# Performance work log

Measured on AMD Instinct MI355X. Metric: run time of the kernel, lower is better.

Reference implementation:

```python
import jax, jax.numpy as jnp
import numpy as np

B, S, D, H = 4, 2048, 1024, 16
HD = D // H
DFF = 4 * D
NUM_LAYERS = 12
RES = 1.0 / float(np.sqrt(NUM_LAYERS))
SCALE = 1.0 / float(np.sqrt(D))  # module divides by sqrt(embed_dim), not head_dim
EPS = 1e-5


def setup_inputs() -> dict:
    key = jax.random.key(0)
    ks = jax.random.split(key, 12)
    s = 0.02
    p = lambda k, shp: (jax.random.normal(k, shp, jnp.float32) * s)
    return {
        "x": jax.random.normal(ks[0], (B, S, D), jnp.float32),
        "Wq": p(ks[1], (D, D)), "bq": jnp.zeros((D,), jnp.float32),
        "Wk": p(ks[2], (D, D)), "bk": jnp.zeros((D,), jnp.float32),
        "Wv": p(ks[3], (D, D)), "bv": jnp.zeros((D,), jnp.float32),
        "Wo": p(ks[4], (D, D)), "bo": jnp.zeros((D,), jnp.float32),
        "g1": jnp.ones((D,), jnp.float32), "be1": jnp.zeros((D,), jnp.float32),
        "g2": jnp.ones((D,), jnp.float32), "be2": jnp.zeros((D,), jnp.float32),
        "W1": p(ks[5], (D, DFF)), "b1": jnp.zeros((DFF,), jnp.float32),
        "W2": p(ks[6], (DFF, D)), "b2": jnp.zeros((D,), jnp.float32),
    }


def _layernorm(x, g, b):
    m = jnp.mean(x, axis=-1, keepdims=True)
    v = jnp.mean((x - m) ** 2, axis=-1, keepdims=True)
    return (x - m) * jax.lax.rsqrt(v + EPS) * g + b


def _attention(x, Wq, bq, Wk, bk, Wv, bv, Wo, bo):
    b, s, d = x.shape
    q = (x @ Wq + bq).reshape(b, s, H, HD)
    k = (x @ Wk + bk).reshape(b, s, H, HD)
    v = (x @ Wv + bv).reshape(b, s, H, HD)
    scores = jnp.einsum('bqhd,bkhd->bhqk', q, k) * SCALE  # [B,H,S,S]
    mask = jnp.tril(jnp.ones((s, s), dtype=bool))
    scores = jnp.where(mask, scores, -jnp.inf)
    attn = jax.nn.softmax(scores, axis=-1)  # dropout_rate=0 -> identity
    out = jnp.einsum('bhqk,bkhd->bqhd', attn, v).reshape(b, s, d)
    return out @ Wo + bo


def reference(x, Wq, bq, Wk, bk, Wv, bv, Wo, bo, g1, be1, g2, be2, W1, b1, W2, b2):
    x = x + RES * _attention(_layernorm(x, g1, be1), Wq, bq, Wk, bk, Wv, bv, Wo, bo)
    h = _layernorm(x, g2, be2)
    ffn = jax.nn.relu(h @ W1 + b1) @ W2 + b2
    x = x + RES * ffn
    return x
```

## Files before the change

kernel.cpp:

```cpp
#include <hip/hip_runtime.h>

typedef unsigned short ushort_t;
typedef unsigned int uint32;
typedef __attribute__((ext_vector_type(4))) float f32x4;
typedef __attribute__((ext_vector_type(8))) short bf16x8;

#define B_   4
#define S_   2048
#define D_   1024
#define H_   16
#define HD_  64
#define DFF_ 4096
#define M_   (B_ * S_)

#define RES_   0.28867513459481287f
#define SCALE_ 0.03125f
#define EPS_   1e-5f
#define LOG2E_ 1.4426950408889634f

__device__ __forceinline__ ushort_t f2bf(float f) {
    union { float f; uint32 u; } c; c.f = f;
    uint32 u = c.u + 0x7fffu + ((c.u >> 16) & 1u);
    return (ushort_t)(u >> 16);
}
__device__ __forceinline__ float bf2f(ushort_t h) {
    union { uint32 u; float f; } c; c.u = ((uint32)h) << 16;
    return c.f;
}
__device__ __forceinline__ float fexp2(float x) {
    float r; asm("v_exp_f32 %0, %1" : "=v"(r) : "v"(x)); return r;
}
__device__ __forceinline__ uint32 cvt_pk_bf16(float lo, float hi) {
    uint32 r;
    asm("v_cvt_pk_bf16_f32 %0, %1, %2" : "=v"(r) : "v"(lo), "v"(hi));
    return r;
}

#define GLDS(src_, dst_)                                                     \
    __builtin_amdgcn_global_load_lds(                                        \
        (const __attribute__((address_space(1))) void*)(src_),               \
        (__attribute__((address_space(3))) void*)(dst_), 16, 0, 0)

__global__ __launch_bounds__(256) void transpose_cast_kernel(
    const float* __restrict__ W, ushort_t* __restrict__ Wt, int K, int N)
{
    __shared__ float tile[32][33];
    const int bx = blockIdx.x * 32;
    const int by = blockIdx.y * 32;
    const int tx = threadIdx.x;
    const int ty = threadIdx.y;
    #pragma unroll
    for (int i = 0; i < 32; i += 8)
        tile[ty + i][tx] = W[(size_t)(by + ty + i) * N + bx + tx];
    __syncthreads();
    #pragma unroll
    for (int i = 0; i < 32; i += 8)
        Wt[(size_t)(bx + ty + i) * K + by + tx] = f2bf(tile[tx][ty + i]);
}

__global__ void concat_bias_kernel(const float* __restrict__ bq,
                                   const float* __restrict__ bk,
                                   const float* __restrict__ bv,
                                   float* __restrict__ bqkv)
{
    int i = blockIdx.x * blockDim.x + threadIdx.x;
    if (i < 3 * D_) {
        float v = (i < D_) ? bq[i] : (i < 2 * D_) ? bk[i - D_] : bv[i - 2 * D_];
        bqkv[i] = v;
    }
}

__global__ __launch_bounds__(256) void ln_kernel(
    const float* __restrict__ x, const float* __restrict__ g,
    const float* __restrict__ be, ushort_t* __restrict__ out)
{
    const int row = blockIdx.x;
    const int t = threadIdx.x;
    const int lane = t & 63;
    const int wave = t >> 6;
    const float4* xr = (const float4*)(x + (size_t)row * D_);
    float4 v = xr[t];
    float s  = v.x + v.y + v.z + v.w;
    float s2 = v.x * v.x + v.y * v.y + v.z * v.z + v.w * v.w;
    #pragma unroll
    for (int off = 32; off; off >>= 1) {
        s  += __shfl_xor(s, off);
        s2 += __shfl_xor(s2, off);
    }
    __shared__ float red[8];
    if (lane == 0) { red[wave * 2] = s; red[wave * 2 + 1] = s2; }
    __syncthreads();
    s  = red[0] + red[2] + red[4] + red[6];
    s2 = red[1] + red[3] + red[5] + red[7];
    const float mean = s * (1.0f / D_);
    const float var  = s2 * (1.0f / D_) - mean * mean;
    const float rstd = rsqrtf(var + EPS_);
    const float4 gv  = ((const float4*)g)[t];
    const float4 bv  = ((const float4*)be)[t];
    ushort_t o[4];
    o[0] = f2bf((v.x - mean) * rstd * gv.x + bv.x);
    o[1] = f2bf((v.y - mean) * rstd * gv.y + bv.y);
    o[2] = f2bf((v.z - mean) * rstd * gv.z + bv.z);
    o[3] = f2bf((v.w - mean) * rstd * gv.w + bv.w);
    *(ushort2*)&out[(size_t)row * D_ + t * 4]     = make_ushort2(o[0], o[1]);
    *(ushort2*)&out[(size_t)row * D_ + t * 4 + 2] = make_ushort2(o[2], o[3]);
}

__global__ __launch_bounds__(256) void vtrans_kernel(
    const ushort_t* __restrict__ qkv, ushort_t* __restrict__ vt)
{
    __shared__ __align__(16) ushort_t T[256 * 64];
    const int tid  = threadIdx.x;
    const int sblk = blockIdx.x & 7;
    const int bh   = blockIdx.x >> 3;
    const int b = bh >> 4, h = bh & 15;
    const ushort_t* src = qkv + (size_t)(b * S_ + sblk * 256) * (3 * D_) + 2 * D_ + h * 64;
    #pragma unroll
    for (int p = 0; p < 8; ++p) {
        const int L = p * 256 + tid;
        const int s = L >> 3, c = L & 7;
        bf16x8 v = *(const bf16x8*)(src + (size_t)s * (3 * D_) + c * 8);
        *(bf16x8*)&T[s * 64 + ((c ^ (s & 7)) << 3)] = v;
    }
    __syncthreads();
    #pragma unroll
    for (int p = 0; p < 8; ++p) {
        const int L = p * 256 + tid;
        const int hd = L >> 5, scn = L & 31;
        ushort_t tmp[8];
        #pragma unroll
        for (int j = 0; j < 8; ++j) {
            const int s = scn * 8 + j;
            tmp[j] = T[s * 64 + (((hd >> 3) ^ (s & 7)) << 3) + (hd & 7)];
        }
        *(bf16x8*)&vt[((size_t)bh * 64 + hd) * S_ + sblk * 256 + scn * 8] =
            *(const bf16x8*)tmp;
    }
}

template <int MODE>
__global__ __launch_bounds__(512, 1) void gemm8p_kernel(
    const ushort_t* __restrict__ A, const ushort_t* __restrict__ Bt,
    const float* __restrict__ bias, const float* __restrict__ res,
    void* __restrict__ Cout, int M, int N, int K, int gx)
{
    __shared__ __align__(16) ushort_t As[2][256 * 64];
    __shared__ __align__(16) ushort_t Bs[2][256 * 64];

    const int tid  = threadIdx.x;
    const int w    = tid >> 6;
    const int lane = tid & 63;
    const int l15  = lane & 15;
    const int g    = lane >> 4;

    const int cpx = gridDim.x >> 3;
    const int swz = (blockIdx.x & 7) * cpx + (blockIdx.x >> 3);
    const int bx = swz % gx, by = swz / gx;
    const int m0 = by * 256, n0 = bx * 256;

    const int wm = (w >> 2) * 128;
    const int wn = (w & 3) * 64;

    const ushort_t* srcA[4];
    const ushort_t* srcB[4];
    int ldsO[4];
    #pragma unroll
    for (int p = 0; p < 4; ++p) {
        const int L = p * 512 + tid;
        const int row = L >> 3;
        const int c = ((L & 7) ^ (row & 7)) << 3;
        srcA[p] = A  + (size_t)(m0 + row) * K + c;
        srcB[p] = Bt + (size_t)(n0 + row) * K + c;
        ldsO[p] = (p * 512 + w * 64) * 8;
    }

    #define LDA(mf_, kk_) (*(const bf16x8*)&As[cur][(wm + (mf_) * 16 + l15) * 64 + \
                  (((((kk_) * 4 + g)) ^ ((wm + (mf_) * 16 + l15) & 7)) << 3)])
    #define LDB(nf_, kk_) (*(const bf16x8*)&Bs[cur][(wn + (nf_) * 16 + l15) * 64 + \
                  (((((kk_) * 4 + g)) ^ ((wn + (nf_) * 16 + l15) & 7)) << 3)])
    #define MM4(base_)                                                         \
        do { _Pragma("unroll")                                                 \
             for (int mf = 0; mf < 4; ++mf)                                    \
                 _Pragma("unroll")                                             \
                 for (int nf = 0; nf < 4; ++nf)                                \
                     acc[(base_) + mf][nf] =                                   \
                         __builtin_amdgcn_mfma_f32_16x16x32_bf16(              \
                             af[mf], bfr[nf], acc[(base_) + mf][nf], 0, 0, 0); \
        } while (0)

    f32x4 acc[8][4] = {};
    const int NT = K >> 6;

    #pragma unroll
    for (int p = 0; p < 4; ++p) GLDS(srcA[p], &As[0][ldsO[p]]);
    #pragma unroll
    for (int p = 0; p < 4; ++p) GLDS(srcB[p], &Bs[0][ldsO[p]]);
    asm volatile("s_waitcnt vmcnt(0)" ::: "memory");
    __builtin_amdgcn_s_barrier();

    for (int t = 0; t < NT; ++t) {
        const int cur = t & 1;
        const int nb  = cur ^ 1;
        const bool more = (t + 1 < NT);
        const size_t koff = (size_t)(t + 1) * 64;

        bf16x8 af[4], bfr[4];

        #pragma unroll
        for (int nf = 0; nf < 4; ++nf) bfr[nf] = LDB(nf, 0);
        #pragma unroll
        for (int mf = 0; mf < 4; ++mf) af[mf] = LDA(mf, 0);
        if (more) {
            #pragma unroll
            for (int p = 0; p < 4; ++p) GLDS(srcA[p] + koff, &As[nb][ldsO[p]]);
        }
        __builtin_amdgcn_s_barrier();
        __builtin_amdgcn_s_setprio(1);
        MM4(0);
        __builtin_amdgcn_s_setprio(0);
        __builtin_amdgcn_s_barrier();

        #pragma unroll
        for (int mf = 0; mf < 4; ++mf) af[mf] = LDA(mf + 4, 0);
        if (more) {
            #pragma unroll
            for (int p = 0; p < 4; ++p) GLDS(srcB[p] + koff, &Bs[nb][ldsO[p]]);
        }
        __builtin_amdgcn_s_barrier();
        __builtin_amdgcn_s_setprio(1);
        MM4(4);
        __builtin_amdgcn_s_setprio(0);
        __builtin_amdgcn_s_barrier();

        #pragma unroll
        for (int nf = 0; nf < 4; ++nf) bfr[nf] = LDB(nf, 1);
        #pragma unroll
        for (int mf = 0; mf < 4; ++mf) af[mf] = LDA(mf, 1);
        __builtin_amdgcn_s_barrier();
        __builtin_amdgcn_s_setprio(1);
        MM4(0);
        __builtin_amdgcn_s_setprio(0);
        __builtin_amdgcn_s_barrier();

        #pragma unroll
        for (int mf = 0; mf < 4; ++mf) af[mf] = LDA(mf + 4, 1);
        __builtin_amdgcn_s_setprio(1);
        MM4(4);
        __builtin_amdgcn_s_setprio(0);
        asm volatile("s_waitcnt vmcnt(0)" ::: "memory");
        __builtin_amdgcn_s_barrier();
    }
    #undef LDA
    #undef LDB
    #undef MM4

    const int rbase = g * 4;
    #pragma unroll
    for (int mf = 0; mf < 8; ++mf) {
        #pragma unroll
        for (int nf = 0; nf < 4; ++nf) {
            const int col = n0 + wn + nf * 16 + l15;
            const float bcol = bias[col];
            #pragma unroll
            for (int r = 0; r < 4; ++r) {
                const int row = m0 + wm + mf * 16 + rbase + r;
                float v = acc[mf][nf][r] + bcol;
                const size_t idx = (size_t)row * N + col;
                if (MODE == 0) {
                    ((ushort_t*)Cout)[idx] = f2bf(v);
                } else if (MODE == 1) {
                    ((ushort_t*)Cout)[idx] = f2bf(fmaxf(v, 0.0f));
                } else {
                    ((float*)Cout)[idx] = res[idx] + RES_ * v;
                }
            }
        }
    }
}

template <int MODE>
__global__ __launch_bounds__(512, 2) void gemmT_kernel(
    const ushort_t* __restrict__ A, const ushort_t* __restrict__ Bt,
    const float* __restrict__ bias, const float* __restrict__ res,
    void* __restrict__ Cout, int M, int N, int K, int gx)
{
    constexpr int LOADS = 3;

    __shared__ __align__(16) ushort_t As[3][128 * 32];
    __shared__ __align__(16) ushort_t Bs[3][256 * 32];

    const int tid  = threadIdx.x;
    const int w    = tid >> 6;
    const int lane = tid & 63;
    const int l15  = lane & 15;
    const int g    = lane >> 4;

    const int cpx = gridDim.x >> 3;
    const int swz = (blockIdx.x & 7) * cpx + (blockIdx.x >> 3);
    const int bx = swz % gx, by = swz / gx;
    const int m0 = by * 128, n0 = bx * 256;

    const int wm = (w >> 2) * 64;
    const int wn = (w & 3) * 64;

    const ushort_t* srcA;
    int ldsA;
    const ushort_t* srcB[2];
    int ldsB[2];
    {
        const int L = tid;
        const int row = L >> 2;
        srcA = A + (size_t)(m0 + row) * K + (((L & 3) ^ ((row >> 1) & 3)) << 3);
        ldsA = (w * 64) * 8;
    }
    #pragma unroll
    for (int p = 0; p < 2; ++p) {
        const int L = p * 512 + tid;
        const int row = L >> 2;
        srcB[p] = Bt + (size_t)(n0 + row) * K + (((L & 3) ^ ((row >> 1) & 3)) << 3);
        ldsB[p] = (p * 512 + w * 64) * 8;
    }

    #define STAGE(koff_, buf_)                                               \
        do {                                                                 \
            GLDS(srcA + (koff_), &As[buf_][ldsA]);                           \
            GLDS(srcB[0] + (koff_), &Bs[buf_][ldsB[0]]);                     \
            GLDS(srcB[1] + (koff_), &Bs[buf_][ldsB[1]]);                     \
        } while (0)

    #define LDA(mf_) (*(const bf16x8*)&As[cur][(wm + (mf_) * 16 + l15) * 32 + \
                        ((g ^ (((wm + (mf_) * 16 + l15) >> 1) & 3)) << 3)])
    #define LDB(nf_) (*(const bf16x8*)&Bs[cur][(wn + (nf_) * 16 + l15) * 32 + \
                        ((g ^ (((wn + (nf_) * 16 + l15) >> 1) & 3)) << 3)])

    f32x4 acc[4][4] = {};
    const int NT = K >> 5;

    STAGE(0, 0);
    STAGE(32, 1);
    asm volatile("s_waitcnt vmcnt(%0)" :: "n"(LOADS) : "memory");
    __builtin_amdgcn_s_barrier();

    for (int t = 0; t < NT; ++t) {
        const int cur = t % 3;
        const bool more = (t + 2 < NT);
        const size_t koff = (size_t)(t + 2) * 32;

        bf16x8 af[4], bfr[4];
        #pragma unroll
        for (int nf = 0; nf < 4; ++nf) bfr[nf] = LDB(nf);
        #pragma unroll
        for (int mf = 0; mf < 4; ++mf) af[mf] = LDA(mf);

        if (more) STAGE(koff, (t + 2) % 3);
        __builtin_amdgcn_s_setprio(1);
        #pragma unroll
        for (int mf = 0; mf < 4; ++mf)
            #pragma unroll
            for (int nf = 0; nf < 4; ++nf)
                acc[mf][nf] = __builtin_amdgcn_mfma_f32_16x16x32_bf16(
                    af[mf], bfr[nf], acc[mf][nf], 0, 0, 0);
        __builtin_amdgcn_s_setprio(0);
        if (more)
            asm volatile("s_waitcnt vmcnt(%0)" :: "n"(LOADS) : "memory");
        else
            asm volatile("s_waitcnt vmcnt(0)" ::: "memory");
        __builtin_amdgcn_s_barrier();
    }
    #undef STAGE
    #undef LDA
    #undef LDB

    const int rbase = g * 4;
    #pragma unroll
    for (int mf = 0; mf < 4; ++mf) {
        #pragma unroll
        for (int nf = 0; nf < 4; ++nf) {
            const int col = n0 + wn + nf * 16 + l15;
            const float bcol = bias[col];
            #pragma unroll
            for (int r = 0; r < 4; ++r) {
                const int row = m0 + wm + mf * 16 + rbase + r;
                float v = acc[mf][nf][r] + bcol;
                const size_t idx = (size_t)row * N + col;
                if (MODE == 0) {
                    ((ushort_t*)Cout)[idx] = f2bf(v);
                } else if (MODE == 1) {
                    ((ushort_t*)Cout)[idx] = f2bf(fmaxf(v, 0.0f));
                } else {
                    ((float*)Cout)[idx] = res[idx] + RES_ * v;
                }
            }
        }
    }
}

__global__ __launch_bounds__(256) void fattn_kernel(
    const ushort_t* __restrict__ qkv, const ushort_t* __restrict__ vtg,
    ushort_t* __restrict__ out)
{
    __shared__ __align__(16) ushort_t Ks[2][64 * 64];
    __shared__ __align__(16) ushort_t Vt[2][64 * 64];
    __shared__ __align__(16) ushort_t Ps[4][16 * 64];

    const int tid  = threadIdx.x;
    const int lane = tid & 63;
    const int w    = tid >> 6;
    const int lin  = blockIdx.x;
    const int xi   = lin >> 6;
    const int bh   = lin & 63;
    const int b = bh >> 4, h = bh & 15;

    const int l15 = lane & 15;
    const int g   = lane >> 4;

    const size_t rs = 3 * D_;
    const ushort_t* Qg = qkv + (size_t)b * S_ * rs + h * HD_;
    const ushort_t* Kg = Qg + D_;
    const ushort_t* Vg = vtg + (size_t)bh * HD_ * S_;

    const int srow = tid >> 3;
    const int sc   = tid & 7;

    #pragma unroll
    for (int half = 0; half < 2; ++half) {
        const int qt = half ? xi : (S_ / 64 - 1) - xi;
        const int q0 = qt * 64;
        const int nkb = qt + 1;

        bf16x8 qf[2];
        {
            const int qrow = q0 + w * 16 + l15;
            #pragma unroll
            for (int kk = 0; kk < 2; ++kk) {
                bf16x8 tq = *(const bf16x8*)(Qg + (size_t)qrow * rs + kk * 32 + g * 8);
                #pragma unroll
                for (int e = 0; e < 8; ++e)
                    tq[e] = (short)f2bf(bf2f((ushort_t)tq[e]) * (SCALE_ * LOG2E_));
                qf[kk] = tq;
            }
        }

        float mrow = -1e30f, lrow = 0.f;
        f32x4 oacc[4] = {};

        bf16x8 kvreg[2][2], vvreg[2][2];
        #pragma unroll
        for (int p = 0; p < 2; ++p) {
            const int row = p * 32 + srow;
            kvreg[0][p] = *(const bf16x8*)(Kg + (size_t)row * rs + sc * 8);
            vvreg[0][p] = *(const bf16x8*)(Vg + (size_t)row * S_ + sc * 8);
        }
        if (nkb > 1) {
            #pragma unroll
            for (int p = 0; p < 2; ++p) {
                const int row = p * 32 + srow;
                kvreg[1][p] = *(const bf16x8*)(Kg + (size_t)(64 + row) * rs + sc * 8);
                vvreg[1][p] = *(const bf16x8*)(Vg + (size_t)row * S_ + 64 + sc * 8);
            }
        }

        int kb = 0;
        for (; kb + 1 < nkb; kb += 2) {
            __syncthreads();
            #pragma unroll
            for (int s = 0; s < 2; ++s)
                #pragma unroll
                for (int p = 0; p < 2; ++p) {
                    const int row = p * 32 + srow;
                    *(bf16x8*)&Ks[s][row * 64 + ((sc ^ (row & 7)) << 3)] = kvreg[s][p];
                    *(bf16x8*)&Vt[s][row * 64 + ((sc ^ (row & 7)) << 3)] = vvreg[s][p];
                }
            if (kb + 2 < nkb) {
                #pragma unroll
                for (int p = 0; p < 2; ++p) {
                    const int row = p * 32 + srow;
                    kvreg[0][p] = *(const bf16x8*)(
                        Kg + (size_t)((kb + 2) * 64 + row) * rs + sc * 8);
                    vvreg[0][p] = *(const bf16x8*)(
                        Vg + (size_t)row * S_ + (kb + 2) * 64 + sc * 8);
                }
            }
            if (kb + 3 < nkb) {
                #pragma unroll
                for (int p = 0; p < 2; ++p) {
                    const int row = p * 32 + srow;
                    kvreg[1][p] = *(const bf16x8*)(
                        Kg + (size_t)((kb + 3) * 64 + row) * rs + sc * 8);
                    vvreg[1][p] = *(const bf16x8*)(
                        Vg + (size_t)row * S_ + (kb + 3) * 64 + sc * 8);
                }
            }
            __syncthreads();

            f32x4 sf0[4] = {}, sf1[4] = {};
            __builtin_amdgcn_s_setprio(1);
            #pragma unroll
            for (int kk = 0; kk < 2; ++kk) {
                const int cc = kk * 4 + g;
                #pragma unroll
                for (int nf = 0; nf < 4; ++nf) {
                    const int keyr = nf * 16 + l15;
                    const int ko = keyr * 64 + ((cc ^ (keyr & 7)) << 3);
                    bf16x8 kf0 = *(const bf16x8*)&Ks[0][ko];
                    bf16x8 kf1 = *(const bf16x8*)&Ks[1][ko];
                    sf0[nf] = __builtin_amdgcn_mfma_f32_16x16x32_bf16(kf0, qf[kk], sf0[nf], 0, 0, 0);
                    sf1[nf] = __builtin_amdgcn_mfma_f32_16x16x32_bf16(kf1, qf[kk], sf1[nf], 0, 0, 0);
                }
            }
            __builtin_amdgcn_s_setprio(0);

            if (kb + 1 == nkb - 1) {
                const int q = q0 + w * 16 + l15;
                #pragma unroll
                for (int nf = 0; nf < 4; ++nf)
                    #pragma unroll
                    for (int r = 0; r < 4; ++r)
                        if ((kb + 1) * 64 + nf * 16 + g * 4 + r > q) sf1[nf][r] = -1e30f;
            }

            float mx = -1e30f;
            #pragma unroll
            for (int nf = 0; nf < 4; ++nf)
                #pragma unroll
                for (int r = 0; r < 4; ++r) {
                    mx = fmaxf(mx, sf0[nf][r]);
                    mx = fmaxf(mx, sf1[nf][r]);
                }
            mx = fmaxf(mx, __shfl_xor(mx, 16));
            mx = fmaxf(mx, __shfl_xor(mx, 32));

            if (!__all(mx - mrow <= 8.0f)) {
                const float mnew = fmaxf(mrow, mx);
                const float corr = fexp2(mrow - mnew);
                mrow = mnew;
                lrow *= corr;
                #pragma unroll
                for (int r = 0; r < 4; ++r) {
                    const float cr = __shfl(corr, g * 4 + r, 16);
                    #pragma unroll
                    for (int nf = 0; nf < 4; ++nf) oacc[nf][r] *= cr;
                }
            }

            float psum = 0.f;
            const int qrow = l15;
            #pragma unroll
            for (int s = 0; s < 2; ++s) {
                const f32x4* sfp = s ? sf1 : sf0;
                #pragma unroll
                for (int nf = 0; nf < 4; ++nf) {
                    const float p0 = fexp2(sfp[nf][0] - mrow);
                    const float p1 = fexp2(sfp[nf][1] - mrow);
                    const float p2 = fexp2(sfp[nf][2] - mrow);
                    const float p3 = fexp2(sfp[nf][3] - mrow);
                    psum += (p0 + p1) + (p2 + p3);
                    uint2 pk = make_uint2(cvt_pk_bf16(p0, p1), cvt_pk_bf16(p2, p3));
                    const int c16 = ((nf << 1) + (g >> 1)) ^ (qrow & 7);
                    *(uint2*)((char*)Ps[w] + qrow * 128 + c16 * 16 + (g & 1) * 8) = pk;
                }
                #pragma unroll
                for (int kk = 0; kk < 2; ++kk) {
                    const int cc = kk * 4 + g;
                    const int c16 = cc ^ (qrow & 7);
                    bf16x8 pa = *(const bf16x8*)((const char*)Ps[w] + qrow * 128 + c16 * 16);
                    __builtin_amdgcn_s_setprio(1);
                    #pragma unroll
                    for (int nf = 0; nf < 4; ++nf) {
                        const int dr = nf * 16 + l15;
                        bf16x8 vf = *(const bf16x8*)&Vt[s][dr * 64 + ((cc ^ (dr & 7)) << 3)];
                        oacc[nf] = __builtin_amdgcn_mfma_f32_16x16x32_bf16(pa, vf, oacc[nf], 0, 0, 0);
                    }
                    __builtin_amdgcn_s_setprio(0);
                }
            }
            psum += __shfl_xor(psum, 16);
            psum += __shfl_xor(psum, 32);
            lrow += psum;
        }

        if (kb < nkb) {
            __syncthreads();
            #pragma unroll
            for (int p = 0; p < 2; ++p) {
                const int row = p * 32 + srow;
                *(bf16x8*)&Ks[0][row * 64 + ((sc ^ (row & 7)) << 3)] = kvreg[0][p];
                *(bf16x8*)&Vt[0][row * 64 + ((sc ^ (row & 7)) << 3)] = vvreg[0][p];
            }
            __syncthreads();

            f32x4 sf0[4] = {};
            __builtin_amdgcn_s_setprio(1);
            #pragma unroll
            for (int kk = 0; kk < 2; ++kk) {
                const int cc = kk * 4 + g;
                #pragma unroll
                for (int nf = 0; nf < 4; ++nf) {
                    const int keyr = nf * 16 + l15;
                    bf16x8 kf = *(const bf16x8*)&Ks[0][keyr * 64 + ((cc ^ (keyr & 7)) << 3)];
                    sf0[nf] = __builtin_amdgcn_mfma_f32_16x16x32_bf16(kf, qf[kk], sf0[nf], 0, 0, 0);
                }
            }
            __builtin_amdgcn_s_setprio(0);

            {
                const int q = q0 + w * 16 + l15;
                #pragma unroll
                for (int nf = 0; nf < 4; ++nf)
                    #pragma unroll
                    for (int r = 0; r < 4; ++r)
                        if (kb * 64 + nf * 16 + g * 4 + r > q) sf0[nf][r] = -1e30f;
            }
            float mx = -1e30f;
            #pragma unroll
            for (int nf = 0; nf < 4; ++nf)
                #pragma unroll
                for (int r = 0; r < 4; ++r) mx = fmaxf(mx, sf0[nf][r]);
            mx = fmaxf(mx, __shfl_xor(mx, 16));
            mx = fmaxf(mx, __shfl_xor(mx, 32));

            if (!__all(mx - mrow <= 8.0f)) {
                const float mnew = fmaxf(mrow, mx);
                const float corr = fexp2(mrow - mnew);
                mrow = mnew;
                lrow *= corr;
                #pragma unroll
                for (int r = 0; r < 4; ++r) {
                    const float cr = __shfl(corr, g * 4 + r, 16);
                    #pragma unroll
                    for (int nf = 0; nf < 4; ++nf) oacc[nf][r] *= cr;
                }
            }

            float psum = 0.f;
            const int qrow = l15;
            #pragma unroll
            for (int nf = 0; nf < 4; ++nf) {
                const float p0 = fexp2(sf0[nf][0] - mrow);
                const float p1 = fexp2(sf0[nf][1] - mrow);
                const float p2 = fexp2(sf0[nf][2] - mrow);
                const float p3 = fexp2(sf0[nf][3] - mrow);
                psum += (p0 + p1) + (p2 + p3);
                uint2 pk = make_uint2(cvt_pk_bf16(p0, p1), cvt_pk_bf16(p2, p3));
                const int c16 = ((nf << 1) + (g >> 1)) ^ (qrow & 7);
                *(uint2*)((char*)Ps[w] + qrow * 128 + c16 * 16 + (g & 1) * 8) = pk;
            }
            psum += __shfl_xor(psum, 16);
            psum += __shfl_xor(psum, 32);
            lrow += psum;

            #pragma unroll
            for (int kk = 0; kk < 2; ++kk) {
                const int cc = kk * 4 + g;
                const int c16 = cc ^ (qrow & 7);
                bf16x8 pa = *(const bf16x8*)((const char*)Ps[w] + qrow * 128 + c16 * 16);
                __builtin_amdgcn_s_setprio(1);
                #pragma unroll
                for (int nf = 0; nf < 4; ++nf) {
                    const int dr = nf * 16 + l15;
                    bf16x8 vf = *(const bf16x8*)&Vt[0][dr * 64 + ((cc ^ (dr & 7)) << 3)];
                    oacc[nf] = __builtin_amdgcn_mfma_f32_16x16x32_bf16(pa, vf, oacc[nf], 0, 0, 0);
                }
                __builtin_amdgcn_s_setprio(0);
            }
        }

        const float linv = 1.0f / lrow;
        #pragma unroll
        for (int r = 0; r < 4; ++r) {
            const float li = __shfl(linv, g * 4 + r, 16);
            const int q = q0 + w * 16 + g * 4 + r;
            ushort_t* op = out + (size_t)(b * S_ + q) * D_ + h * HD_;
            #pragma unroll
            for (int nf = 0; nf < 4; ++nf)
                op[nf * 16 + l15] = f2bf(oacc[nf][r] * li);
        }
    }
}

extern "C" void kernel_launch(void* const* d_in, const int* in_sizes, int n_in,
                              void* d_out, int out_size, void* d_ws, size_t ws_size,
                              hipStream_t stream)
{
    const float* x   = (const float*)d_in[0];
    const float* Wq  = (const float*)d_in[1];
    const float* bq  = (const float*)d_in[2];
    const float* Wk  = (const float*)d_in[3];
    const float* bk  = (const float*)d_in[4];
    const float* Wv  = (const float*)d_in[5];
    const float* bv  = (const float*)d_in[6];
    const float* Wo  = (const float*)d_in[7];
    const float* bo  = (const float*)d_in[8];
    const float* g1  = (const float*)d_in[9];
    const float* be1 = (const float*)d_in[10];
    const float* g2  = (const float*)d_in[11];
    const float* be2 = (const float*)d_in[12];
    const float* W1  = (const float*)d_in[13];
    const float* b1  = (const float*)d_in[14];
    const float* W2  = (const float*)d_in[15];
    const float* b2  = (const float*)d_in[16];
    float* out = (float*)d_out;

    char* ws = (char*)d_ws;
    size_t o = 0;
    auto alloc = [&](size_t bytes) { size_t r = o; o = (o + bytes + 255) & ~(size_t)255; return r; };
    ushort_t* Wqkvt = (ushort_t*)(ws + alloc((size_t)3 * D_ * D_ * 2));
    ushort_t* Wot   = (ushort_t*)(ws + alloc((size_t)D_ * D_ * 2));
    ushort_t* W1t   = (ushort_t*)(ws + alloc((size_t)DFF_ * D_ * 2));
    ushort_t* W2t   = (ushort_t*)(ws + alloc((size_t)D_ * DFF_ * 2));
    float*    bqkv  = (float*)(ws + alloc((size_t)3 * D_ * 4));
    ushort_t* lnbuf = (ushort_t*)(ws + alloc((size_t)M_ * D_ * 2));
    ushort_t* bigbuf= (ushort_t*)(ws + alloc((size_t)M_ * DFF_ * 2));
    ushort_t* attnb = (ushort_t*)(ws + alloc((size_t)M_ * D_ * 2));
    float*    x1    = (float*)(ws + alloc((size_t)M_ * D_ * 4));
    ushort_t* vtbuf = (ushort_t*)(ws + alloc((size_t)M_ * D_ * 2));

    dim3 tblock(32, 8);
    transpose_cast_kernel<<<dim3(D_/32, D_/32), tblock, 0, stream>>>(Wq, Wqkvt,            D_, D_);
    transpose_cast_kernel<<<dim3(D_/32, D_/32), tblock, 0, stream>>>(Wk, Wqkvt + D_*D_,    D_, D_);
    transpose_cast_kernel<<<dim3(D_/32, D_/32), tblock, 0, stream>>>(Wv, Wqkvt + 2*D_*D_,  D_, D_);
    transpose_cast_kernel<<<dim3(D_/32, D_/32), tblock, 0, stream>>>(Wo, Wot,              D_, D_);
    transpose_cast_kernel<<<dim3(DFF_/32, D_/32), tblock, 0, stream>>>(W1, W1t,            D_, DFF_);
    transpose_cast_kernel<<<dim3(D_/32, DFF_/32), tblock, 0, stream>>>(W2, W2t,            DFF_, D_);
    concat_bias_kernel<<<12, 256, 0, stream>>>(bq, bk, bv, bqkv);

    ln_kernel<<<M_, 256, 0, stream>>>(x, g1, be1, lnbuf);
    gemm8p_kernel<0><<<(M_/256)*(3*D_/256), 512, 0, stream>>>(
        lnbuf, Wqkvt, bqkv, nullptr, bigbuf, M_, 3*D_, D_, 3*D_/256);
    vtrans_kernel<<<512, 256, 0, stream>>>(bigbuf, vtbuf);
    fattn_kernel<<<(S_/128) * 64, 256, 0, stream>>>(bigbuf, vtbuf, attnb);
    gemmT_kernel<2><<<(M_/128)*(D_/256), 512, 0, stream>>>(
        attnb, Wot, bo, x, x1, M_, D_, D_, D_/256);
    ln_kernel<<<M_, 256, 0, stream>>>(x1, g2, be2, lnbuf);
    gemm8p_kernel<1><<<(M_/256)*(DFF_/256), 512, 0, stream>>>(
        lnbuf, W1t, b1, nullptr, bigbuf, M_, DFF_, D_, DFF_/256);
    gemmT_kernel<2><<<(M_/128)*(D_/256), 512, 0, stream>>>(
        bigbuf, W2t, b2, x1, out, M_, D_, DFF_, D_/256);
}
```

Baseline: 386.2 us.

## Split GEMM LDS tiles into half-blocks and spread prefetch across four phases

Result: no change. 391.4 us (+1.3%).

```diff
diff --git a/kernel.cpp b/kernel.cpp
--- a/kernel.cpp
+++ b/kernel.cpp
@@ -139,13 +139,13 @@
 }
 
 template <int MODE>
-__global__ __launch_bounds__(512, 1) void gemm8p_kernel(
+__global__ __launch_bounds__(512, 1) void gemm8v_kernel(
     const ushort_t* __restrict__ A, const ushort_t* __restrict__ Bt,
     const float* __restrict__ bias, const float* __restrict__ res,
     void* __restrict__ Cout, int M, int N, int K, int gx)
 {
-    __shared__ __align__(16) ushort_t As[2][256 * 64];
-    __shared__ __align__(16) ushort_t Bs[2][256 * 64];
+    __shared__ __align__(16) ushort_t LdsA[4 * 128 * 64];
+    __shared__ __align__(16) ushort_t LdsB[4 * 128 * 64];
 
     const int tid  = threadIdx.x;
     const int w    = tid >> 6;
@@ -158,26 +158,41 @@
     const int bx = swz % gx, by = swz / gx;
     const int m0 = by * 256, n0 = bx * 256;
 
-    const int wm = (w >> 2) * 128;
+    const int ah = w >> 2;
+    const int bh = (w & 3) >> 1;
+    const int wm = ah * 128;
     const int wn = (w & 3) * 64;
 
     const ushort_t* srcA[4];
     const ushort_t* srcB[4];
-    int ldsO[4];
+    int dstA[4], dstB[4];
     #pragma unroll
     for (int p = 0; p < 4; ++p) {
-        const int L = p * 512 + tid;
-        const int row = L >> 3;
-        const int c = ((L & 7) ^ (row & 7)) << 3;
-        srcA[p] = A  + (size_t)(m0 + row) * K + c;
-        srcB[p] = Bt + (size_t)(n0 + row) * K + c;
-        ldsO[p] = (p * 512 + w * 64) * 8;
-    }
-
-    #define LDA(mf_, kk_) (*(const bf16x8*)&As[cur][(wm + (mf_) * 16 + l15) * 64 + \
-                  (((((kk_) * 4 + g)) ^ ((wm + (mf_) * 16 + l15) & 7)) << 3)])
-    #define LDB(nf_, kk_) (*(const bf16x8*)&Bs[cur][(wn + (nf_) * 16 + l15) * 64 + \
-                  (((((kk_) * 4 + g)) ^ ((wn + (nf_) * 16 + l15) & 7)) << 3)])
+        {
+            const int chunk = (w & 3) * 64 + p * 256 + lane;
+            const int rl = chunk >> 3;
+            srcA[p] = A + (size_t)(m0 + ah * 128 + rl) * K +
+                      (((chunk & 7) ^ (rl & 7)) << 3);
+            dstA[p] = ((w & 3) * 64 + p * 256) * 8;
+        }
+        {
+            const int chunk = ((w >> 2) * 2 + (w & 1)) * 64 + p * 256 + lane;
+            const int rl = chunk >> 3;
+            srcB[p] = Bt + (size_t)(n0 + bh * 128 + rl) * K +
+                      (((chunk & 7) ^ (rl & 7)) << 3);
+            dstB[p] = (((w >> 2) * 2 + (w & 1)) * 64 + p * 256) * 8;
+        }
+    }
+
+    #define SLOTA(t_) ((((t_) & 1) * 2 + ah) * 8192)
+    #define SLOTB(t_) ((((t_) & 1) * 2 + bh) * 8192)
+    #define STG_A(t_, p_)  GLDS(srcA[p_] + (size_t)(t_) * 64, &LdsA[SLOTA(t_) + dstA[p_]])
+    #define STG_B(t_, p_)  GLDS(srcB[p_] + (size_t)(t_) * 64, &LdsB[SLOTB(t_) + dstB[p_]])
+
+    #define LDA(mf_, kk_) (*(const bf16x8*)&LdsA[cA + ((mf_) * 16 + l15) * 64 + \
+                              ((((kk_) * 4 + g) ^ (l15 & 7)) << 3)])
+    #define LDB(nf_, kk_) (*(const bf16x8*)&LdsB[cB + ((w & 1) * 64 + (nf_) * 16 + l15) * 64 + \
+                              ((((kk_) * 4 + g) ^ (l15 & 7)) << 3)])
     #define MM4(base_)                                                         \
         do { _Pragma("unroll")                                                 \
              for (int mf = 0; mf < 4; ++mf)                                    \
@@ -192,17 +207,16 @@
     const int NT = K >> 6;
 
     #pragma unroll
-    for (int p = 0; p < 4; ++p) GLDS(srcA[p], &As[0][ldsO[p]]);
-    #pragma unroll
-    for (int p = 0; p < 4; ++p) GLDS(srcB[p], &Bs[0][ldsO[p]]);
+    for (int p = 0; p < 4; ++p) STG_A(0, p);
+    #pragma unroll
+    for (int p = 0; p < 4; ++p) STG_B(0, p);
     asm volatile("s_waitcnt vmcnt(0)" ::: "memory");
     __builtin_amdgcn_s_barrier();
 
     for (int t = 0; t < NT; ++t) {
-        const int cur = t & 1;
-        const int nb  = cur ^ 1;
+        const int cA = SLOTA(t);
+        const int cB = SLOTB(t);
         const bool more = (t + 1 < NT);
-        const size_t koff = (size_t)(t + 1) * 64;
 
         bf16x8 af[4], bfr[4];
 
@@ -210,10 +224,7 @@
         for (int nf = 0; nf < 4; ++nf) bfr[nf] = LDB(nf, 0);
         #pragma unroll
         for (int mf = 0; mf < 4; ++mf) af[mf] = LDA(mf, 0);
-        if (more) {
-            #pragma unroll
-            for (int p = 0; p < 4; ++p) GLDS(srcA[p] + koff, &As[nb][ldsO[p]]);
-        }
+        if (more) { STG_A(t + 1, 0); STG_A(t + 1, 1); }
         __builtin_amdgcn_s_barrier();
         __builtin_amdgcn_s_setprio(1);
         MM4(0);
@@ -222,10 +233,7 @@
 
         #pragma unroll
         for (int mf = 0; mf < 4; ++mf) af[mf] = LDA(mf + 4, 0);
-        if (more) {
-            #pragma unroll
-            for (int p = 0; p < 4; ++p) GLDS(srcB[p] + koff, &Bs[nb][ldsO[p]]);
-        }
+        if (more) { STG_A(t + 1, 2); STG_A(t + 1, 3); }
         __builtin_amdgcn_s_barrier();
         __builtin_amdgcn_s_setprio(1);
         MM4(4);
@@ -236,6 +244,7 @@
         for (int nf = 0; nf < 4; ++nf) bfr[nf] = LDB(nf, 1);
         #pragma unroll
         for (int mf = 0; mf < 4; ++mf) af[mf] = LDA(mf, 1);
+        if (more) { STG_B(t + 1, 0); STG_B(t + 1, 1); }
         __builtin_amdgcn_s_barrier();
         __builtin_amdgcn_s_setprio(1);
         MM4(0);
@@ -244,12 +253,17 @@
 
         #pragma unroll
         for (int mf = 0; mf < 4; ++mf) af[mf] = LDA(mf + 4, 1);
+        if (more) { STG_B(t + 1, 2); STG_B(t + 1, 3); }
         __builtin_amdgcn_s_setprio(1);
         MM4(4);
         __builtin_amdgcn_s_setprio(0);
         asm volatile("s_waitcnt vmcnt(0)" ::: "memory");
         __builtin_amdgcn_s_barrier();
     }
+    #undef SLOTA
+    #undef SLOTB
+    #undef STG_A
+    #undef STG_B
     #undef LDA
     #undef LDB
     #undef MM4
@@ -725,14 +739,14 @@
     concat_bias_kernel<<<12, 256, 0, stream>>>(bq, bk, bv, bqkv);
 
     ln_kernel<<<M_, 256, 0, stream>>>(x, g1, be1, lnbuf);
-    gemm8p_kernel<0><<<(M_/256)*(3*D_/256), 512, 0, stream>>>(
+    gemm8v_kernel<0><<<(M_/256)*(3*D_/256), 512, 0, stream>>>(
         lnbuf, Wqkvt, bqkv, nullptr, bigbuf, M_, 3*D_, D_, 3*D_/256);
     vtrans_kernel<<<512, 256, 0, stream>>>(bigbuf, vtbuf);
     fattn_kernel<<<(S_/128) * 64, 256, 0, stream>>>(bigbuf, vtbuf, attnb);
     gemmT_kernel<2><<<(M_/128)*(D_/256), 512, 0, stream>>>(
         attnb, Wot, bo, x, x1, M_, D_, D_, D_/256);
     ln_kernel<<<M_, 256, 0, stream>>>(x1, g2, be2, lnbuf);
-    gemm8p_kernel<1><<<(M_/256)*(DFF_/256), 512, 0, stream>>>(
+    gemm8v_kernel<1><<<(M_/256)*(DFF_/256), 512, 0, stream>>>(
         lnbuf, W1t, b1, nullptr, bigbuf, M_, DFF_, D_, DFF_/256);
     gemmT_kernel<2><<<(M_/128)*(D_/256), 512, 0, stream>>>(
         bigbuf, W2t, b2, x1, out, M_, D_, DFF_, D_/256);
```
